# Optimization experiments

Measured on AMD Instinct MI355X. Metric: run time of the kernel, lower is better.

The kernel has to match this reference:

```python
import jax, jax.numpy as jnp
import numpy as np

BATCH, SEQLEN, DMODEL, DSTATE = 8, 2048, 1024, 16


def setup_inputs() -> dict:
    key = jax.random.key(0)
    ks = jax.random.split(key, 6)
    u = jax.random.normal(ks[0], (BATCH, SEQLEN, DMODEL), dtype=jnp.float32)
    # delta (discretization step) is positive in Mamba (post-softplus); sample small positive values
    delta = jax.random.uniform(ks[1], (BATCH, SEQLEN, DMODEL), dtype=jnp.float32, minval=0.001, maxval=0.1)
    # A must be negative so exp(delta*A) is a decay in (0,1)
    A = -jnp.exp(jax.random.normal(ks[2], (DMODEL, DSTATE), dtype=jnp.float32) * 0.5)
    B_mat = jax.random.normal(ks[3], (BATCH, SEQLEN, DSTATE), dtype=jnp.float32)
    C_mat = jax.random.normal(ks[4], (BATCH, SEQLEN, DSTATE), dtype=jnp.float32)
    D_vec = jax.random.normal(ks[5], (DMODEL,), dtype=jnp.float32)
    return {"u": u, "delta": delta, "A": A, "B_mat": B_mat, "C_mat": C_mat, "D_vec": D_vec}


def reference(u, delta, A, B_mat, C_mat, D_vec):
    """Selective scan (Mamba-style):
       h_t = exp(delta_t * A) * h_{t-1} + (delta_t * u_t) * B_t
       y_t = <h_t, C_t> + D * u_t
    u, delta: [B, L, D]; A: [D, N]; B_mat, C_mat: [B, L, N]; D_vec: [D].
    """
    def scan_fn(h, xs):
        u_t, d_t, b_t, c_t = xs                      # [B,D],[B,D],[B,N],[B,N]
        dA = jnp.exp(d_t[..., None] * A)             # [B,D,N] decay
        dBu = (d_t * u_t)[..., None] * b_t[:, None, :]  # [B,D,N] driven input
        h = dA * h + dBu                             # [B,D,N]
        y = jnp.einsum('bdn,bn->bd', h, c_t)         # [B,D]
        return h, y

    h0 = jnp.zeros((u.shape[0], u.shape[2], A.shape[1]), dtype=u.dtype)
    # time-leading layout for lax.scan
    xs = (jnp.swapaxes(u, 0, 1), jnp.swapaxes(delta, 0, 1),
          jnp.swapaxes(B_mat, 0, 1), jnp.swapaxes(C_mat, 0, 1))
    _, ys = jax.lax.scan(scan_fn, h0, xs)            # ys: [L,B,D]
    y = jnp.swapaxes(ys, 0, 1) + u * D_vec           # [B,L,D]
    return y
```

## Files before the change

### kernel.cpp

```cpp
#include <hip/hip_runtime.h>

#define BATCH   8
#define SEQLEN  2048
#define DMODEL  1024
#define DSTATE  16
#define BLOCK   256
#define LOG2E   1.4426950408889634f

template<int NC>
__global__ __launch_bounds__(BLOCK, 8) void ssm_phaseA(
    const float* __restrict__ u,  const float* __restrict__ de,
    const float* __restrict__ A,  const float* __restrict__ Bm,
    float* __restrict__ ws_h, float* __restrict__ ws_d)
{
    constexpr int TC = SEQLEN / NC;
    const int tid = threadIdx.x;
    const int d   = blockIdx.x * BLOCK + tid;
    const int c   = blockIdx.y;
    const int b   = blockIdx.z;
    const int t0  = c * TC;

    float A2[DSTATE];
    #pragma unroll
    for (int n = 0; n < DSTATE; n += 4) {
        float4 a4 = *(const float4*)(A + (size_t)d * DSTATE + n);
        A2[n+0] = a4.x * LOG2E; A2[n+1] = a4.y * LOG2E;
        A2[n+2] = a4.z * LOG2E; A2[n+3] = a4.w * LOG2E;
    }
    float h[DSTATE];
    #pragma unroll
    for (int n = 0; n < DSTATE; ++n) h[n] = 0.f;
    float dsum = 0.f;

    const float* up = u  + (size_t)(b * SEQLEN + t0) * DMODEL + d;
    const float* dp = de + (size_t)(b * SEQLEN + t0) * DMODEL + d;
    const float* brow = Bm + (size_t)(b * SEQLEN + t0) * DSTATE;

    float u0 = up[0], d0 = dp[0];
    float u1 = up[DMODEL], d1 = dp[DMODEL];

    for (int t = 0; t < TC; t += 2) {
        const int i2 = (t + 2 < TC) ? (t + 2) : (TC - 1);
        const int i3 = (t + 3 < TC) ? (t + 3) : (TC - 1);
        float u2 = up[(size_t)i2 * DMODEL], d2 = dp[(size_t)i2 * DMODEL];
        float u3 = up[(size_t)i3 * DMODEL], d3 = dp[(size_t)i3 * DMODEL];

        {
            dsum += d0;
            const float du = d0 * u0;
            #pragma unroll
            for (int n = 0; n < DSTATE; n += 4) {
                float4 b4 = *(const float4*)(brow + (size_t)t * DSTATE + n);
                h[n+0] = __builtin_amdgcn_exp2f(d0 * A2[n+0]) * h[n+0] + du * b4.x;
                h[n+1] = __builtin_amdgcn_exp2f(d0 * A2[n+1]) * h[n+1] + du * b4.y;
                h[n+2] = __builtin_amdgcn_exp2f(d0 * A2[n+2]) * h[n+2] + du * b4.z;
                h[n+3] = __builtin_amdgcn_exp2f(d0 * A2[n+3]) * h[n+3] + du * b4.w;
            }
        }
        {
            dsum += d1;
            const float du = d1 * u1;
            #pragma unroll
            for (int n = 0; n < DSTATE; n += 4) {
                float4 b4 = *(const float4*)(brow + (size_t)(t+1) * DSTATE + n);
                h[n+0] = __builtin_amdgcn_exp2f(d1 * A2[n+0]) * h[n+0] + du * b4.x;
                h[n+1] = __builtin_amdgcn_exp2f(d1 * A2[n+1]) * h[n+1] + du * b4.y;
                h[n+2] = __builtin_amdgcn_exp2f(d1 * A2[n+2]) * h[n+2] + du * b4.z;
                h[n+3] = __builtin_amdgcn_exp2f(d1 * A2[n+3]) * h[n+3] + du * b4.w;
            }
        }
        u0 = u2; d0 = d2; u1 = u3; d1 = d3;
    }

    float* wh = ws_h + (size_t)(b * NC + c) * DSTATE * DMODEL + d;
    #pragma unroll
    for (int n = 0; n < DSTATE; ++n) wh[(size_t)n * DMODEL] = h[n];
    ws_d[(size_t)(b * NC + c) * DMODEL + d] = dsum;
}

template<int NC>
__global__ __launch_bounds__(BLOCK) void ssm_phaseB(
    const float* __restrict__ A,
    float* __restrict__ ws_h, const float* __restrict__ ws_d)
{
    const int gid = blockIdx.x * BLOCK + threadIdx.x;
    const int d  = gid % DMODEL;
    const int bn = gid / DMODEL;
    const int n  = bn % DSTATE;
    const int b  = bn / DSTATE;

    const float a2 = A[(size_t)d * DSTATE + n] * LOG2E;
    float h = 0.f;
    size_t ih = (size_t)b * NC * DSTATE * DMODEL + (size_t)n * DMODEL + d;
    size_t id = (size_t)b * NC * DMODEL + d;

    #pragma unroll 4
    for (int c = 0; c < NC; ++c) {
        float hl = ws_h[ih];
        float ds = ws_d[id];
        ws_h[ih] = h;
        h = __builtin_amdgcn_exp2f(a2 * ds) * h + hl;
        ih += (size_t)DSTATE * DMODEL;
        id += DMODEL;
    }
}

template<int NC>
__global__ __launch_bounds__(BLOCK, 8) void ssm_phaseC(
    const float* __restrict__ u,  const float* __restrict__ de,
    const float* __restrict__ A,  const float* __restrict__ Bm,
    const float* __restrict__ Cm, const float* __restrict__ Dv,
    const float* __restrict__ ws_h, float* __restrict__ y)
{
    constexpr int TC = SEQLEN / NC;
    const int tid = threadIdx.x;
    const int d   = blockIdx.x * BLOCK + tid;
    const int c   = blockIdx.y;
    const int b   = blockIdx.z;
    const int t0  = c * TC;

    float A2[DSTATE];
    #pragma unroll
    for (int n = 0; n < DSTATE; n += 4) {
        float4 a4 = *(const float4*)(A + (size_t)d * DSTATE + n);
        A2[n+0] = a4.x * LOG2E; A2[n+1] = a4.y * LOG2E;
        A2[n+2] = a4.z * LOG2E; A2[n+3] = a4.w * LOG2E;
    }

    float h[DSTATE];
    {
        const float* wh = ws_h + (size_t)(b * NC + c) * DSTATE * DMODEL + d;
        #pragma unroll
        for (int n = 0; n < DSTATE; ++n) h[n] = wh[(size_t)n * DMODEL];
    }

    const float Dd = Dv[d];
    const float* up = u  + (size_t)(b * SEQLEN + t0) * DMODEL + d;
    const float* dp = de + (size_t)(b * SEQLEN + t0) * DMODEL + d;
    const float* brow = Bm + (size_t)(b * SEQLEN + t0) * DSTATE;
    const float* crow = Cm + (size_t)(b * SEQLEN + t0) * DSTATE;
    float* yp = y + (size_t)(b * SEQLEN + t0) * DMODEL + d;

    float u0 = up[0], d0 = dp[0];
    float u1 = up[DMODEL], d1 = dp[DMODEL];

    for (int t = 0; t < TC; t += 2) {
        const int i2 = (t + 2 < TC) ? (t + 2) : (TC - 1);
        const int i3 = (t + 3 < TC) ? (t + 3) : (TC - 1);
        float u2 = up[(size_t)i2 * DMODEL], d2 = dp[(size_t)i2 * DMODEL];
        float u3 = up[(size_t)i3 * DMODEL], d3 = dp[(size_t)i3 * DMODEL];

        {
            const float du = d0 * u0;
            float acc = Dd * u0;
            #pragma unroll
            for (int n = 0; n < DSTATE; n += 4) {
                float4 b4 = *(const float4*)(brow + (size_t)t * DSTATE + n);
                float4 c4 = *(const float4*)(crow + (size_t)t * DSTATE + n);
                h[n+0] = __builtin_amdgcn_exp2f(d0 * A2[n+0]) * h[n+0] + du * b4.x;
                h[n+1] = __builtin_amdgcn_exp2f(d0 * A2[n+1]) * h[n+1] + du * b4.y;
                h[n+2] = __builtin_amdgcn_exp2f(d0 * A2[n+2]) * h[n+2] + du * b4.z;
                h[n+3] = __builtin_amdgcn_exp2f(d0 * A2[n+3]) * h[n+3] + du * b4.w;
                acc += h[n+0] * c4.x; acc += h[n+1] * c4.y;
                acc += h[n+2] * c4.z; acc += h[n+3] * c4.w;
            }
            __builtin_nontemporal_store(acc, yp + (size_t)t * DMODEL);
        }
        {
            const float du = d1 * u1;
            float acc = Dd * u1;
            #pragma unroll
            for (int n = 0; n < DSTATE; n += 4) {
                float4 b4 = *(const float4*)(brow + (size_t)(t+1) * DSTATE + n);
                float4 c4 = *(const float4*)(crow + (size_t)(t+1) * DSTATE + n);
                h[n+0] = __builtin_amdgcn_exp2f(d1 * A2[n+0]) * h[n+0] + du * b4.x;
                h[n+1] = __builtin_amdgcn_exp2f(d1 * A2[n+1]) * h[n+1] + du * b4.y;
                h[n+2] = __builtin_amdgcn_exp2f(d1 * A2[n+2]) * h[n+2] + du * b4.z;
                h[n+3] = __builtin_amdgcn_exp2f(d1 * A2[n+3]) * h[n+3] + du * b4.w;
                acc += h[n+0] * c4.x; acc += h[n+1] * c4.y;
                acc += h[n+2] * c4.z; acc += h[n+3] * c4.w;
            }
            __builtin_nontemporal_store(acc, yp + (size_t)(t+1) * DMODEL);
        }
        u0 = u2; d0 = d2; u1 = u3; d1 = d3;
    }
}

__global__ __launch_bounds__(BLOCK) void ssm_naive(
    const float* __restrict__ u,  const float* __restrict__ de,
    const float* __restrict__ A,  const float* __restrict__ Bm,
    const float* __restrict__ Cm, const float* __restrict__ Dv,
    float* __restrict__ y)
{
    const int tid = threadIdx.x;
    const int d   = blockIdx.x * BLOCK + tid;
    const int b   = blockIdx.z;

    float A2[DSTATE];
    #pragma unroll
    for (int n = 0; n < DSTATE; n += 4) {
        float4 a4 = *(const float4*)(A + (size_t)d * DSTATE + n);
        A2[n+0] = a4.x * LOG2E; A2[n+1] = a4.y * LOG2E;
        A2[n+2] = a4.z * LOG2E; A2[n+3] = a4.w * LOG2E;
    }
    float h[DSTATE];
    #pragma unroll
    for (int n = 0; n < DSTATE; ++n) h[n] = 0.f;
    const float Dd = Dv[d];

    const float* up = u  + (size_t)b * SEQLEN * DMODEL + d;
    const float* dp = de + (size_t)b * SEQLEN * DMODEL + d;
    float* yp = y + (size_t)b * SEQLEN * DMODEL + d;

    for (int t = 0; t < SEQLEN; ++t) {
        float dl = dp[(size_t)t * DMODEL];
        float uu = up[(size_t)t * DMODEL];
        float du  = dl * uu;
        float acc = Dd * uu;
        const float* bp = Bm + (size_t)(b * SEQLEN + t) * DSTATE;
        const float* cp = Cm + (size_t)(b * SEQLEN + t) * DSTATE;
        #pragma unroll
        for (int n = 0; n < DSTATE; n += 4) {
            float4 b4 = *(const float4*)(bp + n);
            float4 c4 = *(const float4*)(cp + n);
            h[n+0] = __builtin_amdgcn_exp2f(dl * A2[n+0]) * h[n+0] + du * b4.x;
            h[n+1] = __builtin_amdgcn_exp2f(dl * A2[n+1]) * h[n+1] + du * b4.y;
            h[n+2] = __builtin_amdgcn_exp2f(dl * A2[n+2]) * h[n+2] + du * b4.z;
            h[n+3] = __builtin_amdgcn_exp2f(dl * A2[n+3]) * h[n+3] + du * b4.w;
            acc += h[n+0] * c4.x;
            acc += h[n+1] * c4.y;
            acc += h[n+2] * c4.z;
            acc += h[n+3] * c4.w;
        }
        yp[(size_t)t * DMODEL] = acc;
    }
}

template<int NC>
static void launch_chunked(const float* u, const float* de, const float* A,
                           const float* Bm, const float* Cm, const float* Dv,
                           float* ws_h, float* ws_d, float* y, hipStream_t stream) {
    dim3 grid(DMODEL / BLOCK, NC, BATCH);
    ssm_phaseA<NC><<<grid, BLOCK, 0, stream>>>(u, de, A, Bm, ws_h, ws_d);
    dim3 gridB((BATCH * DSTATE * DMODEL) / BLOCK, 1, 1);
    ssm_phaseB<NC><<<gridB, BLOCK, 0, stream>>>(A, ws_h, ws_d);
    ssm_phaseC<NC><<<grid, BLOCK, 0, stream>>>(u, de, A, Bm, Cm, Dv, ws_h, y);
}

extern "C" void kernel_launch(void* const* d_in, const int* in_sizes, int n_in,
                              void* d_out, int out_size, void* d_ws, size_t ws_size,
                              hipStream_t stream) {
    const float* u  = (const float*)d_in[0];
    const float* de = (const float*)d_in[1];
    const float* A  = (const float*)d_in[2];
    const float* Bm = (const float*)d_in[3];
    const float* Cm = (const float*)d_in[4];
    const float* Dv = (const float*)d_in[5];
    float* y = (float*)d_out;

    auto need = [](int nc) {
        return ((size_t)BATCH * nc * DSTATE * DMODEL +
                (size_t)BATCH * nc * DMODEL) * sizeof(float);
    };

    if (ws_size >= need(64)) {
        float* ws_h = (float*)d_ws;
        float* ws_d = ws_h + (size_t)BATCH * 64 * DSTATE * DMODEL;
        launch_chunked<64>(u, de, A, Bm, Cm, Dv, ws_h, ws_d, y, stream);
    } else if (ws_size >= need(16)) {
        float* ws_h = (float*)d_ws;
        float* ws_d = ws_h + (size_t)BATCH * 16 * DSTATE * DMODEL;
        launch_chunked<16>(u, de, A, Bm, Cm, Dv, ws_h, ws_d, y, stream);
    } else {
        dim3 grid(DMODEL / BLOCK, 1, BATCH);
        ssm_naive<<<grid, BLOCK, 0, stream>>>(u, de, A, Bm, Cm, Dv, y);
    }
}
```

Baseline: 113.9 us.

## Stage B/C rows in LDS, fully unroll chunk loop, and try 128 chunks

Phases A and C now copy the chunk's B (and C) rows into shared memory once per block, then read them from LDS instead of issuing per-thread global broadcast loads on every timestep. The time loop is fully unrolled. The chunk count rises to 128 when the workspace allows, which shortens each chunk and adds parallelism but doubles the inter-chunk state traffic in phase B. The phase C occupancy hint drops to 7 blocks per CU. Full unrolling and the extra LDS could raise register and code-size pressure, and if the workspace is too small for 128 chunks the code falls back to 64 rather than 16.

```diff
diff --git a/kernel.cpp b/kernel.cpp
--- a/kernel.cpp
+++ b/kernel.cpp
@@ -14,12 +14,17 @@
     float* __restrict__ ws_h, float* __restrict__ ws_d)
 {
     constexpr int TC = SEQLEN / NC;
+    __shared__ float sB[TC * DSTATE];
     const int tid = threadIdx.x;
     const int d   = blockIdx.x * BLOCK + tid;
     const int c   = blockIdx.y;
     const int b   = blockIdx.z;
     const int t0  = c * TC;
 
+    for (int i = tid; i < TC * DSTATE / 4; i += BLOCK)
+        ((float4*)sB)[i] =
+            ((const float4*)(Bm + (size_t)(b * SEQLEN + t0) * DSTATE))[i];
+
     float A2[DSTATE];
     #pragma unroll
     for (int n = 0; n < DSTATE; n += 4) {
@@ -34,11 +39,13 @@
 
     const float* up = u  + (size_t)(b * SEQLEN + t0) * DMODEL + d;
     const float* dp = de + (size_t)(b * SEQLEN + t0) * DMODEL + d;
-    const float* brow = Bm + (size_t)(b * SEQLEN + t0) * DSTATE;
+
+    __syncthreads();
 
     float u0 = up[0], d0 = dp[0];
     float u1 = up[DMODEL], d1 = dp[DMODEL];
 
+    #pragma unroll
     for (int t = 0; t < TC; t += 2) {
         const int i2 = (t + 2 < TC) ? (t + 2) : (TC - 1);
         const int i3 = (t + 3 < TC) ? (t + 3) : (TC - 1);
@@ -50,7 +57,7 @@
             const float du = d0 * u0;
             #pragma unroll
             for (int n = 0; n < DSTATE; n += 4) {
-                float4 b4 = *(const float4*)(brow + (size_t)t * DSTATE + n);
+                float4 b4 = *(const float4*)(sB + t * DSTATE + n);
                 h[n+0] = __builtin_amdgcn_exp2f(d0 * A2[n+0]) * h[n+0] + du * b4.x;
                 h[n+1] = __builtin_amdgcn_exp2f(d0 * A2[n+1]) * h[n+1] + du * b4.y;
                 h[n+2] = __builtin_amdgcn_exp2f(d0 * A2[n+2]) * h[n+2] + du * b4.z;
@@ -62,7 +69,7 @@
             const float du = d1 * u1;
             #pragma unroll
             for (int n = 0; n < DSTATE; n += 4) {
-                float4 b4 = *(const float4*)(brow + (size_t)(t+1) * DSTATE + n);
+                float4 b4 = *(const float4*)(sB + (t+1) * DSTATE + n);
                 h[n+0] = __builtin_amdgcn_exp2f(d1 * A2[n+0]) * h[n+0] + du * b4.x;
                 h[n+1] = __builtin_amdgcn_exp2f(d1 * A2[n+1]) * h[n+1] + du * b4.y;
                 h[n+2] = __builtin_amdgcn_exp2f(d1 * A2[n+2]) * h[n+2] + du * b4.z;
@@ -106,19 +113,28 @@
 }
 
 template<int NC>
-__global__ __launch_bounds__(BLOCK, 8) void ssm_phaseC(
+__global__ __launch_bounds__(BLOCK, 7) void ssm_phaseC(
     const float* __restrict__ u,  const float* __restrict__ de,
     const float* __restrict__ A,  const float* __restrict__ Bm,
     const float* __restrict__ Cm, const float* __restrict__ Dv,
     const float* __restrict__ ws_h, float* __restrict__ y)
 {
     constexpr int TC = SEQLEN / NC;
+    __shared__ float sB[TC * DSTATE];
+    __shared__ float sC[TC * DSTATE];
     const int tid = threadIdx.x;
     const int d   = blockIdx.x * BLOCK + tid;
     const int c   = blockIdx.y;
     const int b   = blockIdx.z;
     const int t0  = c * TC;
 
+    for (int i = tid; i < TC * DSTATE / 4; i += BLOCK)
+        ((float4*)sB)[i] =
+            ((const float4*)(Bm + (size_t)(b * SEQLEN + t0) * DSTATE))[i];
+    for (int i = tid; i < TC * DSTATE / 4; i += BLOCK)
+        ((float4*)sC)[i] =
+            ((const float4*)(Cm + (size_t)(b * SEQLEN + t0) * DSTATE))[i];
+
     float A2[DSTATE];
     #pragma unroll
     for (int n = 0; n < DSTATE; n += 4) {
@@ -137,13 +153,14 @@
     const float Dd = Dv[d];
     const float* up = u  + (size_t)(b * SEQLEN + t0) * DMODEL + d;
     const float* dp = de + (size_t)(b * SEQLEN + t0) * DMODEL + d;
-    const float* brow = Bm + (size_t)(b * SEQLEN + t0) * DSTATE;
-    const float* crow = Cm + (size_t)(b * SEQLEN + t0) * DSTATE;
     float* yp = y + (size_t)(b * SEQLEN + t0) * DMODEL + d;
+
+    __syncthreads();
 
     float u0 = up[0], d0 = dp[0];
     float u1 = up[DMODEL], d1 = dp[DMODEL];
 
+    #pragma unroll
     for (int t = 0; t < TC; t += 2) {
         const int i2 = (t + 2 < TC) ? (t + 2) : (TC - 1);
         const int i3 = (t + 3 < TC) ? (t + 3) : (TC - 1);
@@ -155,8 +172,8 @@
             float acc = Dd * u0;
             #pragma unroll
             for (int n = 0; n < DSTATE; n += 4) {
-                float4 b4 = *(const float4*)(brow + (size_t)t * DSTATE + n);
-                float4 c4 = *(const float4*)(crow + (size_t)t * DSTATE + n);
+                float4 b4 = *(const float4*)(sB + t * DSTATE + n);
+                float4 c4 = *(const float4*)(sC + t * DSTATE + n);
                 h[n+0] = __builtin_amdgcn_exp2f(d0 * A2[n+0]) * h[n+0] + du * b4.x;
                 h[n+1] = __builtin_amdgcn_exp2f(d0 * A2[n+1]) * h[n+1] + du * b4.y;
                 h[n+2] = __builtin_amdgcn_exp2f(d0 * A2[n+2]) * h[n+2] + du * b4.z;
@@ -171,8 +188,8 @@
             float acc = Dd * u1;
             #pragma unroll
             for (int n = 0; n < DSTATE; n += 4) {
-                float4 b4 = *(const float4*)(brow + (size_t)(t+1) * DSTATE + n);
-                float4 c4 = *(const float4*)(crow + (size_t)(t+1) * DSTATE + n);
+                float4 b4 = *(const float4*)(sB + (t+1) * DSTATE + n);
+                float4 c4 = *(const float4*)(sC + (t+1) * DSTATE + n);
                 h[n+0] = __builtin_amdgcn_exp2f(d1 * A2[n+0]) * h[n+0] + du * b4.x;
                 h[n+1] = __builtin_amdgcn_exp2f(d1 * A2[n+1]) * h[n+1] + du * b4.y;
                 h[n+2] = __builtin_amdgcn_exp2f(d1 * A2[n+2]) * h[n+2] + du * b4.z;
@@ -239,7 +256,9 @@
 template<int NC>
 static void launch_chunked(const float* u, const float* de, const float* A,
                            const float* Bm, const float* Cm, const float* Dv,
-                           float* ws_h, float* ws_d, float* y, hipStream_t stream) {
+                           float* ws, float* y, hipStream_t stream) {
+    float* ws_h = ws;
+    float* ws_d = ws_h + (size_t)BATCH * NC * DSTATE * DMODEL;
     dim3 grid(DMODEL / BLOCK, NC, BATCH);
     ssm_phaseA<NC><<<grid, BLOCK, 0, stream>>>(u, de, A, Bm, ws_h, ws_d);
     dim3 gridB((BATCH * DSTATE * DMODEL) / BLOCK, 1, 1);
@@ -263,14 +282,10 @@
                 (size_t)BATCH * nc * DMODEL) * sizeof(float);
     };
 
-    if (ws_size >= need(64)) {
-        float* ws_h = (float*)d_ws;
-        float* ws_d = ws_h + (size_t)BATCH * 64 * DSTATE * DMODEL;
-        launch_chunked<64>(u, de, A, Bm, Cm, Dv, ws_h, ws_d, y, stream);
-    } else if (ws_size >= need(16)) {
-        float* ws_h = (float*)d_ws;
-        float* ws_d = ws_h + (size_t)BATCH * 16 * DSTATE * DMODEL;
-        launch_chunked<16>(u, de, A, Bm, Cm, Dv, ws_h, ws_d, y, stream);
+    if (ws_size >= need(128)) {
+        launch_chunked<128>(u, de, A, Bm, Cm, Dv, (float*)d_ws, y, stream);
+    } else if (ws_size >= need(64)) {
+        launch_chunked<64>(u, de, A, Bm, Cm, Dv, (float*)d_ws, y, stream);
     } else {
         dim3 grid(DMODEL / BLOCK, 1, BATCH);
         ssm_naive<<<grid, BLOCK, 0, stream>>>(u, de, A, Bm, Cm, Dv, y);
```

New measurement: 118.0 us. 1.04x slower.
